# Kernel optimization log

Hardware: AMD Instinct MI355X
Metric: run time of the kernel (lower is better)

Reference implementation:

```python
import jax, jax.numpy as jnp
import numpy as np

GAMMA = 0.01   # module default gamma
STEP = 10      # forward subsamples time axis with x[::10]
BIG = 1e10     # finite stand-in for +inf boundary (exp(-BIG/gamma) underflows to 0 exactly)


def _softdtw(D, gamma):
    """Batched soft-DTW DP over cost matrices D: (B, N, M) -> (B,).
    Anti-diagonal wavefront: lax.scan over the 2*max(N,M)-1 diagonals,
    each diagonal updated fully vectorized (mirrors compute_softdtw_cuda).
    """
    B, N, M = D.shape
    inv_g = 1.0 / gamma
    # padded R, boundaries at BIG (acts as +inf), R[:,0,0] = 0
    R0 = jnp.full((B, N + 2, M + 2), BIG, dtype=D.dtype).at[:, 0, 0].set(0.0)
    ii = jnp.arange(1, N + 1)  # padded row indices on a diagonal

    def step(R, p):
        jj = p + 2 - ii                      # i + j = p + 2 in padded coords
        valid = (jj >= 1) & (jj <= M)
        jc = jnp.clip(jj, 1, M)
        r0 = -R[:, ii - 1, jc - 1] * inv_g   # diag neighbor
        r1 = -R[:, ii - 1, jc] * inv_g       # up neighbor
        r2 = -R[:, ii, jc - 1] * inv_g       # left neighbor
        rmax = jnp.maximum(jnp.maximum(r0, r1), r2)
        rsum = jnp.exp(r0 - rmax) + jnp.exp(r1 - rmax) + jnp.exp(r2 - rmax)
        softmin = -gamma * (jnp.log(rsum) + rmax)
        new = D[:, ii - 1, jc - 1] + softmin
        R = R.at[:, ii, jc].set(jnp.where(valid[None, :], new, R[:, ii, jc]))
        return R, None

    R, _ = jax.lax.scan(step, R0, jnp.arange(N + M - 1))
    return R[:, N, M]


def _loss(x, y):
    # x, y: (nt, nr, nc). Subsample time by STEP; treat each (r, c) trace as a
    # batch-1, dim-1 sequence; sum soft-DTW values over all nr*nc traces.
    xs = x[::STEP]                      # (L, nr, nc)
    ys = y[::STEP]
    L = xs.shape[0]
    X = xs.reshape(L, -1).T             # (B, L), B = nr*nc
    Y = ys.reshape(L, -1).T
    D = (X[:, :, None] - Y[:, None, :]) ** 2  # squared-Euclidean cost, d=1
    return jnp.sum(_softdtw(D, GAMMA)).reshape(1)


def setup_inputs() -> dict:
    key = jax.random.key(0)
    k1, k2 = jax.random.split(key)
    x = jax.random.normal(k1, (2048, 128, 2), dtype=jnp.float32)
    y = jax.random.normal(k2, (2048, 128, 2), dtype=jnp.float32)
    return {"x": x, "y": y}


def reference(x, y):
    return _loss(x, y)
```

## Files before the change

### kernel.cpp

```cpp
#include <hip/hip_runtime.h>

#define STEP 10
#define NCH  256
#define CSCL (-144.2695041f)
#define GLN2 (-0.00693147181f)
#define BIGP (-1.442695041e12f)
#define YOFF 64
#define YLDS 384
#define BNDSZ 472
#define NW   4

__device__ __forceinline__ float fexp2(float x){ float r; asm("v_exp_f32 %0, %1" : "=v"(r) : "v"(x)); return r; }
__device__ __forceinline__ float flog2(float x){ float r; asm("v_log_f32 %0, %1" : "=v"(r) : "v"(x)); return r; }

__device__ __forceinline__ float dpp_shr1(float src){
    int s = __builtin_bit_cast(int, src);
    int r = __builtin_amdgcn_update_dpp(0, s, 0x138 , 0xF, 0xF, true);
    return __builtin_bit_cast(float, r);
}

__device__ __forceinline__ float dpcell(float up2, float up, float left, float qq) {
    float m  = fmaxf(fmaxf(up2, up), left);
    float lo = fminf(fminf(up2, up), left);
    float md = __builtin_amdgcn_fmed3f(up2, up, left);
    float e  = fexp2(lo - m) + fexp2(md - m) + 1.0f;
    float mq = m + qq;
    return flog2(e) + mq;
}

__global__ __launch_bounds__(256, 1)
void softdtw_wave(const float* __restrict__ x, const float* __restrict__ y,
                  float* __restrict__ ws, int N) {
    const int b = blockIdx.x;
    const int t = threadIdx.x;
    const int l = t & 63;
    const int w = t >> 6;

    __shared__ __align__(16) float Ys[YLDS];
    __shared__ float bnd[NW - 1][BNDSZ];
    __shared__ int prog[NW - 1];

    for (int j = t; j < YLDS; j += 256) Ys[j] = 0.f;
    float* bf = &bnd[0][0];
    for (int j = t; j < (NW - 1) * BNDSZ; j += 256) bf[j] = BIGP;
    if (t < NW - 1) prog[t] = 0;
    __syncthreads();
    for (int j = t; j < N; j += 256) Ys[YOFF + j] = y[j * STEP * NCH + b];
    __syncthreads();

    const int i = 64 * w + l + 1;
    const float xv = (i <= N) ? x[(i - 1) * STEP * NCH + b] : 0.f;

    float sp = BIGP, bp = BIGP;
    float bq = (t == 0) ? 0.0f : BIGP;

    const int smax = 2 * N;
    const int sb0  = 64 * w + 2;
    const int myrows = (64 * (w + 1) < N) ? 64 * (w + 1) : N;
    const int NG     = (myrows + N - sb0 + 1 + 7) >> 3;
    const bool prod = (w < NW - 1);
    const bool cons = (w > 0);
    const int prows = (64 * w < N) ? 64 * w : N;
    const int pNG   = (prows + N - (sb0 - 64) + 1 + 7) >> 3;
    const int progFinal = (sb0 - 64) + 8 * pNG - 1;

    const float* yb = Ys + (YOFF - l);
    const float* bb = cons ? bnd[w - 1] : bnd[0];

    #define POLL(NEED) do {                                               \
        const int need_ = min((NEED), progFinal);                         \
        while (__hip_atomic_load(&prog[w - 1], __ATOMIC_ACQUIRE,          \
                                 __HIP_MEMORY_SCOPE_WORKGROUP) < need_)   \
            __builtin_amdgcn_s_sleep(1);                                  \
    } while (0)

    float q0,q1,q2,q3,q4,q5,q6,q7;
    float h0,h1,h2,h3,h4,h5,h6,h7;
    {
        float a0=yb[0],a1=yb[1],a2=yb[2],a3=yb[3];
        float a4=yb[4],a5=yb[5],a6=yb[6],a7=yb[7];
        if (cons) {
            POLL(sb0 + 7);
            if (l == 0) bp = bb[sb0 - 1];
            h0=bb[sb0+0]; h1=bb[sb0+1]; h2=bb[sb0+2]; h3=bb[sb0+3];
            h4=bb[sb0+4]; h5=bb[sb0+5]; h6=bb[sb0+6]; h7=bb[sb0+7];
        } else {
            h0=h1=h2=h3=h4=h5=h6=h7 = BIGP;
        }
        float d;
        d=xv-a0; q0=d*CSCL*d;  d=xv-a1; q1=d*CSCL*d;
        d=xv-a2; q2=d*CSCL*d;  d=xv-a3; q3=d*CSCL*d;
        d=xv-a4; q4=d*CSCL*d;  d=xv-a5; q5=d*CSCL*d;
        d=xv-a6; q6=d*CSCL*d;  d=xv-a7; q7=d*CSCL*d;
    }

    #define STEPJ(QQ, HJ, CJ, J) do {                              \
        CJ = dpcell(bq, bp, sp, (QQ));                             \
        float sh = dpp_shr1(CJ);                                   \
        bq = bp;                                                   \
        bp = (l == 0) ? (HJ) : sh;                                 \
        sp = CJ;                                                   \
        if (sb + (J) == smax && i == N) ws[b] = CJ * GLN2;         \
    } while (0)

    for (int m = 0; m < NG; ++m) {
        const int sb = sb0 + 8 * m;
        float c0,c1,c2,c3,c4,c5,c6,c7;
        STEPJ(q0, h0, c0, 0); STEPJ(q1, h1, c1, 1);
        STEPJ(q2, h2, c2, 2); STEPJ(q3, h3, c3, 3);
        STEPJ(q4, h4, c4, 4); STEPJ(q5, h5, c5, 5);
        STEPJ(q6, h6, c6, 6); STEPJ(q7, h7, c7, 7);

        if (prod && l == 63) {
            float* bw = &bnd[w][sb];
            bw[0]=c0; bw[1]=c1; bw[2]=c2; bw[3]=c3;
            bw[4]=c4; bw[5]=c5; bw[6]=c6; bw[7]=c7;
            __hip_atomic_store(&prog[w], sb + 7, __ATOMIC_RELEASE,
                               __HIP_MEMORY_SCOPE_WORKGROUP);
        }

        if (m + 1 < NG) {
            const float* yn = yb + 8 * (m + 1);
            float a0=yn[0],a1=yn[1],a2=yn[2],a3=yn[3];
            float a4=yn[4],a5=yn[5],a6=yn[6],a7=yn[7];
            if (cons) {
                POLL(sb + 15);
                h0=bb[sb+8];  h1=bb[sb+9];  h2=bb[sb+10]; h3=bb[sb+11];
                h4=bb[sb+12]; h5=bb[sb+13]; h6=bb[sb+14]; h7=bb[sb+15];
            }
            float d;
            d=xv-a0; q0=d*CSCL*d;  d=xv-a1; q1=d*CSCL*d;
            d=xv-a2; q2=d*CSCL*d;  d=xv-a3; q3=d*CSCL*d;
            d=xv-a4; q4=d*CSCL*d;  d=xv-a5; q5=d*CSCL*d;
            d=xv-a6; q6=d*CSCL*d;  d=xv-a7; q7=d*CSCL*d;
        }
    }
    #undef STEPJ
    #undef POLL
}

__global__ __launch_bounds__(256)
void reduce256(const float* __restrict__ ws, float* __restrict__ out) {
    const int tid = threadIdx.x;
    float v = ws[tid];
    #pragma unroll
    for (int off = 32; off > 0; off >>= 1)
        v += __shfl_down(v, off, 64);
    __shared__ float partial[4];
    if ((tid & 63) == 0) partial[tid >> 6] = v;
    __syncthreads();
    if (tid == 0) out[0] = (partial[0] + partial[1]) + (partial[2] + partial[3]);
}

extern "C" void kernel_launch(void* const* d_in, const int* in_sizes, int n_in,
                              void* d_out, int out_size, void* d_ws, size_t ws_size,
                              hipStream_t stream) {
    const float* x = (const float*)d_in[0];
    const float* y = (const float*)d_in[1];
    float* out = (float*)d_out;
    float* ws  = (float*)d_ws;

    const int T = in_sizes[0] / NCH;
    const int L = (T + STEP - 1) / STEP;

    softdtw_wave<<<dim3(NCH), dim3(256), 0, stream>>>(x, y, ws, L);
    reduce256<<<dim3(1), dim3(256), 0, stream>>>(ws, out);
}
```

Measured before the change: 38.17 us.

## Process two traces per block to interleave independent DP chains

Each workgroup now runs two independent soft-DTW problems (channels 2b and 2b+1) side by side, interleaving their per-cell computations so the serial exp/log/DPP dependency chain of one trace can overlap with the other. The grid halves to 128 blocks. The DPP shift now takes the lane-0 boundary value as its old operand, which removes a separate select. In exchange it uses twice the registers and LDS per block, and only 128 of the GPU's CUs get work.

```diff
diff --git a/kernel.cpp b/kernel.cpp
--- a/kernel.cpp
+++ b/kernel.cpp
@@ -13,9 +13,10 @@
 __device__ __forceinline__ float fexp2(float x){ float r; asm("v_exp_f32 %0, %1" : "=v"(r) : "v"(x)); return r; }
 __device__ __forceinline__ float flog2(float x){ float r; asm("v_log_f32 %0, %1" : "=v"(r) : "v"(x)); return r; }
 
-__device__ __forceinline__ float dpp_shr1(float src){
+__device__ __forceinline__ float dpp_shr1_sel(float h, float src){
+    int o = __builtin_bit_cast(int, h);
     int s = __builtin_bit_cast(int, src);
-    int r = __builtin_amdgcn_update_dpp(0, s, 0x138 , 0xF, 0xF, true);
+    int r = __builtin_amdgcn_update_dpp(o, s, 0x138 , 0xF, 0xF, false);
     return __builtin_bit_cast(float, r);
 }
 
@@ -31,28 +32,33 @@
 __global__ __launch_bounds__(256, 1)
 void softdtw_wave(const float* __restrict__ x, const float* __restrict__ y,
                   float* __restrict__ ws, int N) {
-    const int b = blockIdx.x;
+    const int bA = blockIdx.x * 2;
+    const int bB = bA + 1;
     const int t = threadIdx.x;
     const int l = t & 63;
     const int w = t >> 6;
 
-    __shared__ __align__(16) float Ys[YLDS];
-    __shared__ float bnd[NW - 1][BNDSZ];
+    __shared__ __align__(16) float YsA[YLDS], YsB[YLDS];
+    __shared__ float bndA[NW - 1][BNDSZ], bndB[NW - 1][BNDSZ];
     __shared__ int prog[NW - 1];
 
-    for (int j = t; j < YLDS; j += 256) Ys[j] = 0.f;
-    float* bf = &bnd[0][0];
-    for (int j = t; j < (NW - 1) * BNDSZ; j += 256) bf[j] = BIGP;
+    for (int j = t; j < YLDS; j += 256) { YsA[j] = 0.f; YsB[j] = 0.f; }
+    float* bfA = &bndA[0][0]; float* bfB = &bndB[0][0];
+    for (int j = t; j < (NW - 1) * BNDSZ; j += 256) { bfA[j] = BIGP; bfB[j] = BIGP; }
     if (t < NW - 1) prog[t] = 0;
     __syncthreads();
-    for (int j = t; j < N; j += 256) Ys[YOFF + j] = y[j * STEP * NCH + b];
+    for (int j = t; j < N; j += 256) {
+        YsA[YOFF + j] = y[j * STEP * NCH + bA];
+        YsB[YOFF + j] = y[j * STEP * NCH + bB];
+    }
     __syncthreads();
 
     const int i = 64 * w + l + 1;
-    const float xv = (i <= N) ? x[(i - 1) * STEP * NCH + b] : 0.f;
-
-    float sp = BIGP, bp = BIGP;
-    float bq = (t == 0) ? 0.0f : BIGP;
+    const float xvA = (i <= N) ? x[(i - 1) * STEP * NCH + bA] : 0.f;
+    const float xvB = (i <= N) ? x[(i - 1) * STEP * NCH + bB] : 0.f;
+
+    float spA = BIGP, bpA = BIGP, bqA = (t == 0) ? 0.0f : BIGP;
+    float spB = BIGP, bpB = BIGP, bqB = (t == 0) ? 0.0f : BIGP;
 
     const int smax = 2 * N;
     const int sb0  = 64 * w + 2;
@@ -64,8 +70,10 @@
     const int pNG   = (prows + N - (sb0 - 64) + 1 + 7) >> 3;
     const int progFinal = (sb0 - 64) + 8 * pNG - 1;
 
-    const float* yb = Ys + (YOFF - l);
-    const float* bb = cons ? bnd[w - 1] : bnd[0];
+    const float* ybA = YsA + (YOFF - l);
+    const float* ybB = YsB + (YOFF - l);
+    const float* bbA = cons ? bndA[w - 1] : bndA[0];
+    const float* bbB = cons ? bndB[w - 1] : bndB[0];
 
     #define POLL(NEED) do {                                               \
         const int need_ = min((NEED), progFinal);                         \
@@ -74,68 +82,97 @@
             __builtin_amdgcn_s_sleep(1);                                  \
     } while (0)
 
-    float q0,q1,q2,q3,q4,q5,q6,q7;
-    float h0,h1,h2,h3,h4,h5,h6,h7;
+    float qA0,qA1,qA2,qA3,qA4,qA5,qA6,qA7, qB0,qB1,qB2,qB3,qB4,qB5,qB6,qB7;
+    float hA0,hA1,hA2,hA3,hA4,hA5,hA6,hA7, hB0,hB1,hB2,hB3,hB4,hB5,hB6,hB7;
     {
-        float a0=yb[0],a1=yb[1],a2=yb[2],a3=yb[3];
-        float a4=yb[4],a5=yb[5],a6=yb[6],a7=yb[7];
+        float a0=ybA[0],a1=ybA[1],a2=ybA[2],a3=ybA[3];
+        float a4=ybA[4],a5=ybA[5],a6=ybA[6],a7=ybA[7];
+        float e0=ybB[0],e1=ybB[1],e2=ybB[2],e3=ybB[3];
+        float e4=ybB[4],e5=ybB[5],e6=ybB[6],e7=ybB[7];
         if (cons) {
             POLL(sb0 + 7);
-            if (l == 0) bp = bb[sb0 - 1];
-            h0=bb[sb0+0]; h1=bb[sb0+1]; h2=bb[sb0+2]; h3=bb[sb0+3];
-            h4=bb[sb0+4]; h5=bb[sb0+5]; h6=bb[sb0+6]; h7=bb[sb0+7];
+            if (l == 0) { bpA = bbA[sb0 - 1]; bpB = bbB[sb0 - 1]; }
+            hA0=bbA[sb0+0]; hA1=bbA[sb0+1]; hA2=bbA[sb0+2]; hA3=bbA[sb0+3];
+            hA4=bbA[sb0+4]; hA5=bbA[sb0+5]; hA6=bbA[sb0+6]; hA7=bbA[sb0+7];
+            hB0=bbB[sb0+0]; hB1=bbB[sb0+1]; hB2=bbB[sb0+2]; hB3=bbB[sb0+3];
+            hB4=bbB[sb0+4]; hB5=bbB[sb0+5]; hB6=bbB[sb0+6]; hB7=bbB[sb0+7];
         } else {
-            h0=h1=h2=h3=h4=h5=h6=h7 = BIGP;
+            hA0=hA1=hA2=hA3=hA4=hA5=hA6=hA7 = BIGP;
+            hB0=hB1=hB2=hB3=hB4=hB5=hB6=hB7 = BIGP;
         }
         float d;
-        d=xv-a0; q0=d*CSCL*d;  d=xv-a1; q1=d*CSCL*d;
-        d=xv-a2; q2=d*CSCL*d;  d=xv-a3; q3=d*CSCL*d;
-        d=xv-a4; q4=d*CSCL*d;  d=xv-a5; q5=d*CSCL*d;
-        d=xv-a6; q6=d*CSCL*d;  d=xv-a7; q7=d*CSCL*d;
+        d=xvA-a0; qA0=d*CSCL*d;  d=xvA-a1; qA1=d*CSCL*d;
+        d=xvA-a2; qA2=d*CSCL*d;  d=xvA-a3; qA3=d*CSCL*d;
+        d=xvA-a4; qA4=d*CSCL*d;  d=xvA-a5; qA5=d*CSCL*d;
+        d=xvA-a6; qA6=d*CSCL*d;  d=xvA-a7; qA7=d*CSCL*d;
+        d=xvB-e0; qB0=d*CSCL*d;  d=xvB-e1; qB1=d*CSCL*d;
+        d=xvB-e2; qB2=d*CSCL*d;  d=xvB-e3; qB3=d*CSCL*d;
+        d=xvB-e4; qB4=d*CSCL*d;  d=xvB-e5; qB5=d*CSCL*d;
+        d=xvB-e6; qB6=d*CSCL*d;  d=xvB-e7; qB7=d*CSCL*d;
     }
 
-    #define STEPJ(QQ, HJ, CJ, J) do {                              \
-        CJ = dpcell(bq, bp, sp, (QQ));                             \
-        float sh = dpp_shr1(CJ);                                   \
-        bq = bp;                                                   \
-        bp = (l == 0) ? (HJ) : sh;                                 \
-        sp = CJ;                                                   \
-        if (sb + (J) == smax && i == N) ws[b] = CJ * GLN2;         \
+    #define STEPJ2(QA, HA, CA, QB, HB, CB, J) do {                 \
+        CA = dpcell(bqA, bpA, spA, (QA));                          \
+        CB = dpcell(bqB, bpB, spB, (QB));                          \
+        float nA = dpp_shr1_sel((HA), CA);                         \
+        float nB = dpp_shr1_sel((HB), CB);                         \
+        bqA = bpA; bpA = nA; spA = CA;                             \
+        bqB = bpB; bpB = nB; spB = CB;                             \
+        if (sb + (J) == smax && i == N) {                          \
+            ws[bA] = CA * GLN2; ws[bB] = CB * GLN2;                \
+        }                                                          \
     } while (0)
 
     for (int m = 0; m < NG; ++m) {
         const int sb = sb0 + 8 * m;
-        float c0,c1,c2,c3,c4,c5,c6,c7;
-        STEPJ(q0, h0, c0, 0); STEPJ(q1, h1, c1, 1);
-        STEPJ(q2, h2, c2, 2); STEPJ(q3, h3, c3, 3);
-        STEPJ(q4, h4, c4, 4); STEPJ(q5, h5, c5, 5);
-        STEPJ(q6, h6, c6, 6); STEPJ(q7, h7, c7, 7);
+        float cA0,cA1,cA2,cA3,cA4,cA5,cA6,cA7;
+        float cB0,cB1,cB2,cB3,cB4,cB5,cB6,cB7;
+        STEPJ2(qA0,hA0,cA0, qB0,hB0,cB0, 0);
+        STEPJ2(qA1,hA1,cA1, qB1,hB1,cB1, 1);
+        STEPJ2(qA2,hA2,cA2, qB2,hB2,cB2, 2);
+        STEPJ2(qA3,hA3,cA3, qB3,hB3,cB3, 3);
+        STEPJ2(qA4,hA4,cA4, qB4,hB4,cB4, 4);
+        STEPJ2(qA5,hA5,cA5, qB5,hB5,cB5, 5);
+        STEPJ2(qA6,hA6,cA6, qB6,hB6,cB6, 6);
+        STEPJ2(qA7,hA7,cA7, qB7,hB7,cB7, 7);
 
         if (prod && l == 63) {
-            float* bw = &bnd[w][sb];
-            bw[0]=c0; bw[1]=c1; bw[2]=c2; bw[3]=c3;
-            bw[4]=c4; bw[5]=c5; bw[6]=c6; bw[7]=c7;
+            float* bwA = &bndA[w][sb];
+            bwA[0]=cA0; bwA[1]=cA1; bwA[2]=cA2; bwA[3]=cA3;
+            bwA[4]=cA4; bwA[5]=cA5; bwA[6]=cA6; bwA[7]=cA7;
+            float* bwB = &bndB[w][sb];
+            bwB[0]=cB0; bwB[1]=cB1; bwB[2]=cB2; bwB[3]=cB3;
+            bwB[4]=cB4; bwB[5]=cB5; bwB[6]=cB6; bwB[7]=cB7;
             __hip_atomic_store(&prog[w], sb + 7, __ATOMIC_RELEASE,
                                __HIP_MEMORY_SCOPE_WORKGROUP);
         }
 
         if (m + 1 < NG) {
-            const float* yn = yb + 8 * (m + 1);
-            float a0=yn[0],a1=yn[1],a2=yn[2],a3=yn[3];
-            float a4=yn[4],a5=yn[5],a6=yn[6],a7=yn[7];
+            const float* ynA = ybA + 8 * (m + 1);
+            const float* ynB = ybB + 8 * (m + 1);
+            float a0=ynA[0],a1=ynA[1],a2=ynA[2],a3=ynA[3];
+            float a4=ynA[4],a5=ynA[5],a6=ynA[6],a7=ynA[7];
+            float e0=ynB[0],e1=ynB[1],e2=ynB[2],e3=ynB[3];
+            float e4=ynB[4],e5=ynB[5],e6=ynB[6],e7=ynB[7];
             if (cons) {
                 POLL(sb + 15);
-                h0=bb[sb+8];  h1=bb[sb+9];  h2=bb[sb+10]; h3=bb[sb+11];
-                h4=bb[sb+12]; h5=bb[sb+13]; h6=bb[sb+14]; h7=bb[sb+15];
+                hA0=bbA[sb+8];  hA1=bbA[sb+9];  hA2=bbA[sb+10]; hA3=bbA[sb+11];
+                hA4=bbA[sb+12]; hA5=bbA[sb+13]; hA6=bbA[sb+14]; hA7=bbA[sb+15];
+                hB0=bbB[sb+8];  hB1=bbB[sb+9];  hB2=bbB[sb+10]; hB3=bbB[sb+11];
+                hB4=bbB[sb+12]; hB5=bbB[sb+13]; hB6=bbB[sb+14]; hB7=bbB[sb+15];
             }
             float d;
-            d=xv-a0; q0=d*CSCL*d;  d=xv-a1; q1=d*CSCL*d;
-            d=xv-a2; q2=d*CSCL*d;  d=xv-a3; q3=d*CSCL*d;
-            d=xv-a4; q4=d*CSCL*d;  d=xv-a5; q5=d*CSCL*d;
-            d=xv-a6; q6=d*CSCL*d;  d=xv-a7; q7=d*CSCL*d;
+            d=xvA-a0; qA0=d*CSCL*d;  d=xvA-a1; qA1=d*CSCL*d;
+            d=xvA-a2; qA2=d*CSCL*d;  d=xvA-a3; qA3=d*CSCL*d;
+            d=xvA-a4; qA4=d*CSCL*d;  d=xvA-a5; qA5=d*CSCL*d;
+            d=xvA-a6; qA6=d*CSCL*d;  d=xvA-a7; qA7=d*CSCL*d;
+            d=xvB-e0; qB0=d*CSCL*d;  d=xvB-e1; qB1=d*CSCL*d;
+            d=xvB-e2; qB2=d*CSCL*d;  d=xvB-e3; qB3=d*CSCL*d;
+            d=xvB-e4; qB4=d*CSCL*d;  d=xvB-e5; qB5=d*CSCL*d;
+            d=xvB-e6; qB6=d*CSCL*d;  d=xvB-e7; qB7=d*CSCL*d;
         }
     }
-    #undef STEPJ
+    #undef STEPJ2
     #undef POLL
 }
 
@@ -163,6 +200,6 @@
     const int T = in_sizes[0] / NCH;
     const int L = (T + STEP - 1) / STEP;
 
-    softdtw_wave<<<dim3(NCH), dim3(256), 0, stream>>>(x, y, ws, L);
+    softdtw_wave<<<dim3(NCH / 2), dim3(256), 0, stream>>>(x, y, ws, L);
     reduce256<<<dim3(1), dim3(256), 0, stream>>>(ws, out);
 }
```

Measured after the change: 53.72 us. +40.7%, slower.

## Double-buffer boundary/Y loads, fold reduction into last block, early progress signals

Applied to the files above, without the earlier changes.

The DP loop is unrolled by two with ping-pong register sets, so Y values and boundary values for the next group are loaded while the current group computes, and the cost term is computed inline per cell. The DPP shift now takes the boundary value as its 'old' operand with bound_ctrl off, which removes the lane-0 select. Producers publish progress before writing their boundary values, and a sentinel is set at the end. The separate reduction kernel is replaced by an atomic counter where the last block sums the results, which adds a memset launch. The early progress store may let consumers read before the data is written, since the index it publishes looks like it refers only to earlier, already-written groups.

```diff
diff --git a/kernel.cpp b/kernel.cpp
--- a/kernel.cpp
+++ b/kernel.cpp
@@ -13,9 +13,10 @@
 __device__ __forceinline__ float fexp2(float x){ float r; asm("v_exp_f32 %0, %1" : "=v"(r) : "v"(x)); return r; }
 __device__ __forceinline__ float flog2(float x){ float r; asm("v_log_f32 %0, %1" : "=v"(r) : "v"(x)); return r; }
 
-__device__ __forceinline__ float dpp_shr1(float src){
+__device__ __forceinline__ float dpp_shr1_sel(float h, float src){
+    int o = __builtin_bit_cast(int, h);
     int s = __builtin_bit_cast(int, src);
-    int r = __builtin_amdgcn_update_dpp(0, s, 0x138 , 0xF, 0xF, true);
+    int r = __builtin_amdgcn_update_dpp(o, s, 0x138 , 0xF, 0xF, false);
     return __builtin_bit_cast(float, r);
 }
 
@@ -28,9 +29,14 @@
     return flog2(e) + mq;
 }
 
+#define PIN8(A0,A1,A2,A3,A4,A5,A6,A7) \
+    asm volatile("" : "+v"(A0),"+v"(A1),"+v"(A2),"+v"(A3), \
+                      "+v"(A4),"+v"(A5),"+v"(A6),"+v"(A7))
+
 __global__ __launch_bounds__(256, 1)
 void softdtw_wave(const float* __restrict__ x, const float* __restrict__ y,
-                  float* __restrict__ ws, int N) {
+                  float* __restrict__ ws, int* __restrict__ cnt,
+                  float* __restrict__ out, int N) {
     const int b = blockIdx.x;
     const int t = threadIdx.x;
     const int l = t & 63;
@@ -39,6 +45,8 @@
     __shared__ __align__(16) float Ys[YLDS];
     __shared__ float bnd[NW - 1][BNDSZ];
     __shared__ int prog[NW - 1];
+    __shared__ float res_s;
+    __shared__ int last_s;
 
     for (int j = t; j < YLDS; j += 256) Ys[j] = 0.f;
     float* bf = &bnd[0][0];
@@ -64,7 +72,7 @@
     const int pNG   = (prows + N - (sb0 - 64) + 1 + 7) >> 3;
     const int progFinal = (sb0 - 64) + 8 * pNG - 1;
 
-    const float* yb = Ys + (YOFF - l);
+    const float* yrow = Ys + (YOFF - l);
     const float* bb = cons ? bnd[w - 1] : bnd[0];
 
     #define POLL(NEED) do {                                               \
@@ -74,82 +82,135 @@
             __builtin_amdgcn_s_sleep(1);                                  \
     } while (0)
 
-    float q0,q1,q2,q3,q4,q5,q6,q7;
-    float h0,h1,h2,h3,h4,h5,h6,h7;
-    {
-        float a0=yb[0],a1=yb[1],a2=yb[2],a3=yb[3];
-        float a4=yb[4],a5=yb[5],a6=yb[6],a7=yb[7];
-        if (cons) {
-            POLL(sb0 + 7);
-            if (l == 0) bp = bb[sb0 - 1];
-            h0=bb[sb0+0]; h1=bb[sb0+1]; h2=bb[sb0+2]; h3=bb[sb0+3];
-            h4=bb[sb0+4]; h5=bb[sb0+5]; h6=bb[sb0+6]; h7=bb[sb0+7];
-        } else {
-            h0=h1=h2=h3=h4=h5=h6=h7 = BIGP;
+    float ya0,ya1,ya2,ya3,ya4,ya5,ya6,ya7, hb0,hb1,hb2,hb3,hb4,hb5,hb6,hb7;
+    float yB0,yB1,yB2,yB3,yB4,yB5,yB6,yB7, ha0,ha1,ha2,ha3,ha4,ha5,ha6,ha7;
+    ya0=yrow[0]; ya1=yrow[1]; ya2=yrow[2]; ya3=yrow[3];
+    ya4=yrow[4]; ya5=yrow[5]; ya6=yrow[6]; ya7=yrow[7];
+    yB0=yrow[8]; yB1=yrow[9]; yB2=yrow[10]; yB3=yrow[11];
+    yB4=yrow[12]; yB5=yrow[13]; yB6=yrow[14]; yB7=yrow[15];
+    if (cons) {
+        POLL(sb0 + 15);
+        if (l == 0) bp = bb[sb0 - 1];
+        ha0=bb[sb0+0]; ha1=bb[sb0+1]; ha2=bb[sb0+2]; ha3=bb[sb0+3];
+        ha4=bb[sb0+4]; ha5=bb[sb0+5]; ha6=bb[sb0+6]; ha7=bb[sb0+7];
+        hb0=bb[sb0+8]; hb1=bb[sb0+9]; hb2=bb[sb0+10]; hb3=bb[sb0+11];
+        hb4=bb[sb0+12]; hb5=bb[sb0+13]; hb6=bb[sb0+14]; hb7=bb[sb0+15];
+    } else {
+        ha0=ha1=ha2=ha3=ha4=ha5=ha6=ha7 = BIGP;
+        hb0=hb1=hb2=hb3=hb4=hb5=hb6=hb7 = BIGP;
+    }
+    PIN8(ya0,ya1,ya2,ya3,ya4,ya5,ya6,ya7);
+    PIN8(ha0,ha1,ha2,ha3,ha4,ha5,ha6,ha7);
+
+    #define STEPJ(YV, HJ, CJ, J) do {                              \
+        float d_ = xv - (YV);                                      \
+        float q_ = d_ * CSCL * d_;                                 \
+        CJ = dpcell(bq, bp, sp, q_);                               \
+        float n_ = dpp_shr1_sel((HJ), CJ);                         \
+        bq = bp; bp = n_; sp = CJ;                                 \
+        if (sb + (J) == smax && i == N) res_s = CJ * GLN2;         \
+    } while (0)
+
+    int m = 0;
+    for (; m + 1 < NG; m += 2) {
+        {
+            const int sb = sb0 + 8 * m;
+            float c0,c1,c2,c3,c4,c5,c6,c7;
+            STEPJ(ya0,ha0,c0,0); STEPJ(ya1,ha1,c1,1);
+            STEPJ(ya2,ha2,c2,2); STEPJ(ya3,ha3,c3,3);
+            STEPJ(ya4,ha4,c4,4); STEPJ(ya5,ha5,c5,5);
+            STEPJ(ya6,ha6,c6,6); STEPJ(ya7,ha7,c7,7);
+            if (prod && l == 63) {
+                __hip_atomic_store(&prog[w], sb - 1, __ATOMIC_RELEASE,
+                                   __HIP_MEMORY_SCOPE_WORKGROUP);
+                float* bw = &bnd[w][sb];
+                bw[0]=c0; bw[1]=c1; bw[2]=c2; bw[3]=c3;
+                bw[4]=c4; bw[5]=c5; bw[6]=c6; bw[7]=c7;
+            }
+            if (m + 2 < NG) {
+                if (cons) {
+                    POLL(sb0 + 8*(m+2) + 7);
+                    const float* hh = &bb[sb0 + 8*(m+2)];
+                    ha0=hh[0]; ha1=hh[1]; ha2=hh[2]; ha3=hh[3];
+                    ha4=hh[4]; ha5=hh[5]; ha6=hh[6]; ha7=hh[7];
+                }
+                const float* yn = yrow + 8*(m+2);
+                ya0=yn[0]; ya1=yn[1]; ya2=yn[2]; ya3=yn[3];
+                ya4=yn[4]; ya5=yn[5]; ya6=yn[6]; ya7=yn[7];
+            }
+            PIN8(yB0,yB1,yB2,yB3,yB4,yB5,yB6,yB7);
+            PIN8(hb0,hb1,hb2,hb3,hb4,hb5,hb6,hb7);
         }
-        float d;
-        d=xv-a0; q0=d*CSCL*d;  d=xv-a1; q1=d*CSCL*d;
-        d=xv-a2; q2=d*CSCL*d;  d=xv-a3; q3=d*CSCL*d;
-        d=xv-a4; q4=d*CSCL*d;  d=xv-a5; q5=d*CSCL*d;
-        d=xv-a6; q6=d*CSCL*d;  d=xv-a7; q7=d*CSCL*d;
-    }
-
-    #define STEPJ(QQ, HJ, CJ, J) do {                              \
-        CJ = dpcell(bq, bp, sp, (QQ));                             \
-        float sh = dpp_shr1(CJ);                                   \
-        bq = bp;                                                   \
-        bp = (l == 0) ? (HJ) : sh;                                 \
-        sp = CJ;                                                   \
-        if (sb + (J) == smax && i == N) ws[b] = CJ * GLN2;         \
-    } while (0)
-
-    for (int m = 0; m < NG; ++m) {
+        {
+            const int sb = sb0 + 8 * (m + 1);
+            float c0,c1,c2,c3,c4,c5,c6,c7;
+            STEPJ(yB0,hb0,c0,0); STEPJ(yB1,hb1,c1,1);
+            STEPJ(yB2,hb2,c2,2); STEPJ(yB3,hb3,c3,3);
+            STEPJ(yB4,hb4,c4,4); STEPJ(yB5,hb5,c5,5);
+            STEPJ(yB6,hb6,c6,6); STEPJ(yB7,hb7,c7,7);
+            if (prod && l == 63) {
+                __hip_atomic_store(&prog[w], sb - 1, __ATOMIC_RELEASE,
+                                   __HIP_MEMORY_SCOPE_WORKGROUP);
+                float* bw = &bnd[w][sb];
+                bw[0]=c0; bw[1]=c1; bw[2]=c2; bw[3]=c3;
+                bw[4]=c4; bw[5]=c5; bw[6]=c6; bw[7]=c7;
+            }
+            if (m + 3 < NG) {
+                if (cons) {
+                    POLL(sb0 + 8*(m+3) + 7);
+                    const float* hh = &bb[sb0 + 8*(m+3)];
+                    hb0=hh[0]; hb1=hh[1]; hb2=hh[2]; hb3=hh[3];
+                    hb4=hh[4]; hb5=hh[5]; hb6=hh[6]; hb7=hh[7];
+                }
+                const float* yn = yrow + 8*(m+3);
+                yB0=yn[0]; yB1=yn[1]; yB2=yn[2]; yB3=yn[3];
+                yB4=yn[4]; yB5=yn[5]; yB6=yn[6]; yB7=yn[7];
+            }
+            PIN8(ya0,ya1,ya2,ya3,ya4,ya5,ya6,ya7);
+            PIN8(ha0,ha1,ha2,ha3,ha4,ha5,ha6,ha7);
+        }
+    }
+    if (m < NG) {
         const int sb = sb0 + 8 * m;
         float c0,c1,c2,c3,c4,c5,c6,c7;
-        STEPJ(q0, h0, c0, 0); STEPJ(q1, h1, c1, 1);
-        STEPJ(q2, h2, c2, 2); STEPJ(q3, h3, c3, 3);
-        STEPJ(q4, h4, c4, 4); STEPJ(q5, h5, c5, 5);
-        STEPJ(q6, h6, c6, 6); STEPJ(q7, h7, c7, 7);
-
+        STEPJ(ya0,ha0,c0,0); STEPJ(ya1,ha1,c1,1);
+        STEPJ(ya2,ha2,c2,2); STEPJ(ya3,ha3,c3,3);
+        STEPJ(ya4,ha4,c4,4); STEPJ(ya5,ha5,c5,5);
+        STEPJ(ya6,ha6,c6,6); STEPJ(ya7,ha7,c7,7);
         if (prod && l == 63) {
+            __hip_atomic_store(&prog[w], sb - 1, __ATOMIC_RELEASE,
+                               __HIP_MEMORY_SCOPE_WORKGROUP);
             float* bw = &bnd[w][sb];
             bw[0]=c0; bw[1]=c1; bw[2]=c2; bw[3]=c3;
             bw[4]=c4; bw[5]=c5; bw[6]=c6; bw[7]=c7;
-            __hip_atomic_store(&prog[w], sb + 7, __ATOMIC_RELEASE,
-                               __HIP_MEMORY_SCOPE_WORKGROUP);
         }
-
-        if (m + 1 < NG) {
-            const float* yn = yb + 8 * (m + 1);
-            float a0=yn[0],a1=yn[1],a2=yn[2],a3=yn[3];
-            float a4=yn[4],a5=yn[5],a6=yn[6],a7=yn[7];
-            if (cons) {
-                POLL(sb + 15);
-                h0=bb[sb+8];  h1=bb[sb+9];  h2=bb[sb+10]; h3=bb[sb+11];
-                h4=bb[sb+12]; h5=bb[sb+13]; h6=bb[sb+14]; h7=bb[sb+15];
-            }
-            float d;
-            d=xv-a0; q0=d*CSCL*d;  d=xv-a1; q1=d*CSCL*d;
-            d=xv-a2; q2=d*CSCL*d;  d=xv-a3; q3=d*CSCL*d;
-            d=xv-a4; q4=d*CSCL*d;  d=xv-a5; q5=d*CSCL*d;
-            d=xv-a6; q6=d*CSCL*d;  d=xv-a7; q7=d*CSCL*d;
-        }
-    }
+    }
+    if (prod && l == 63)
+        __hip_atomic_store(&prog[w], 0x3FFFFFFF, __ATOMIC_RELEASE,
+                           __HIP_MEMORY_SCOPE_WORKGROUP);
     #undef STEPJ
     #undef POLL
-}
-
-__global__ __launch_bounds__(256)
-void reduce256(const float* __restrict__ ws, float* __restrict__ out) {
-    const int tid = threadIdx.x;
-    float v = ws[tid];
-    #pragma unroll
-    for (int off = 32; off > 0; off >>= 1)
-        v += __shfl_down(v, off, 64);
-    __shared__ float partial[4];
-    if ((tid & 63) == 0) partial[tid >> 6] = v;
-    __syncthreads();
-    if (tid == 0) out[0] = (partial[0] + partial[1]) + (partial[2] + partial[3]);
+
+    __syncthreads();
+    if (t == 0) {
+        __hip_atomic_store(&ws[b], res_s, __ATOMIC_RELEASE,
+                           __HIP_MEMORY_SCOPE_AGENT);
+        int prev = __hip_atomic_fetch_add(cnt, 1, __ATOMIC_ACQ_REL,
+                                          __HIP_MEMORY_SCOPE_AGENT);
+        last_s = (prev == NCH - 1);
+    }
+    __syncthreads();
+    if (last_s) {
+        float v = __hip_atomic_load(&ws[t], __ATOMIC_RELAXED,
+                                    __HIP_MEMORY_SCOPE_AGENT);
+        #pragma unroll
+        for (int off = 32; off > 0; off >>= 1)
+            v += __shfl_down(v, off, 64);
+        __shared__ float partial[4];
+        if ((t & 63) == 0) partial[t >> 6] = v;
+        __syncthreads();
+        if (t == 0) out[0] = (partial[0] + partial[1]) + (partial[2] + partial[3]);
+    }
 }
 
 extern "C" void kernel_launch(void* const* d_in, const int* in_sizes, int n_in,
@@ -159,10 +220,11 @@
     const float* y = (const float*)d_in[1];
     float* out = (float*)d_out;
     float* ws  = (float*)d_ws;
+    int*   cnt = (int*)(ws + NCH);
 
     const int T = in_sizes[0] / NCH;
     const int L = (T + STEP - 1) / STEP;
 
-    softdtw_wave<<<dim3(NCH), dim3(256), 0, stream>>>(x, y, ws, L);
-    reduce256<<<dim3(1), dim3(256), 0, stream>>>(ws, out);
-}
+    hipMemsetAsync(cnt, 0, sizeof(int), stream);
+    softdtw_wave<<<dim3(NCH), dim3(256), 0, stream>>>(x, y, ws, cnt, out, L);
+}
```

Measured after the change: 48.26 us. +26.4%, slower.

## Split soft-DTW rows across eight waves of 26 rows each

Applied to the files above, without the earlier changes.

The wavefront pipeline goes from 4 waves of 64 rows to 8 waves per block, each owning a 26-row stripe. Stripes are mapped so consecutive stages sit on different SIMDs. The lane-0 boundary select is folded into the DPP move by using the old-value operand with bound_ctrl off, which removes a per-cell v_cndmask. The goal is a shorter critical path: less pipeline fill per stage and fewer serial cells per wave, at the cost of more producer/consumer handoffs and idle lanes (38 of 64 lanes do redundant work).

```diff
diff --git a/kernel.cpp b/kernel.cpp
--- a/kernel.cpp
+++ b/kernel.cpp
@@ -7,15 +7,17 @@
 #define BIGP (-1.442695041e12f)
 #define YOFF 64
 #define YLDS 384
-#define BNDSZ 472
-#define NW   4
+#define BNDSZ 424
+#define NWAVE 8
+#define SROW 26
 
 __device__ __forceinline__ float fexp2(float x){ float r; asm("v_exp_f32 %0, %1" : "=v"(r) : "v"(x)); return r; }
 __device__ __forceinline__ float flog2(float x){ float r; asm("v_log_f32 %0, %1" : "=v"(r) : "v"(x)); return r; }
 
-__device__ __forceinline__ float dpp_shr1(float src){
+__device__ __forceinline__ float dpp_shr1_sel(float h, float src){
+    int o = __builtin_bit_cast(int, h);
     int s = __builtin_bit_cast(int, src);
-    int r = __builtin_amdgcn_update_dpp(0, s, 0x138 , 0xF, 0xF, true);
+    int r = __builtin_amdgcn_update_dpp(o, s, 0x138 , 0xF, 0xF, false);
     return __builtin_bit_cast(float, r);
 }
 
@@ -28,48 +30,51 @@
     return flog2(e) + mq;
 }
 
-__global__ __launch_bounds__(256, 1)
+__global__ __launch_bounds__(512, 1)
 void softdtw_wave(const float* __restrict__ x, const float* __restrict__ y,
                   float* __restrict__ ws, int N) {
     const int b = blockIdx.x;
     const int t = threadIdx.x;
     const int l = t & 63;
     const int w = t >> 6;
+    const int stg = ((w & 3) << 1) | (w >> 2);
 
     __shared__ __align__(16) float Ys[YLDS];
-    __shared__ float bnd[NW - 1][BNDSZ];
-    __shared__ int prog[NW - 1];
+    __shared__ float bnd[NWAVE - 1][BNDSZ];
+    __shared__ int prog[NWAVE - 1];
 
-    for (int j = t; j < YLDS; j += 256) Ys[j] = 0.f;
+    for (int j = t; j < YLDS; j += 512) Ys[j] = 0.f;
     float* bf = &bnd[0][0];
-    for (int j = t; j < (NW - 1) * BNDSZ; j += 256) bf[j] = BIGP;
-    if (t < NW - 1) prog[t] = 0;
+    for (int j = t; j < (NWAVE - 1) * BNDSZ; j += 512) bf[j] = BIGP;
+    if (t < NWAVE - 1) prog[t] = 0;
     __syncthreads();
-    for (int j = t; j < N; j += 256) Ys[YOFF + j] = y[j * STEP * NCH + b];
+    for (int j = t; j < N; j += 512) Ys[YOFF + j] = y[j * STEP * NCH + b];
     __syncthreads();
 
-    const int i = 64 * w + l + 1;
+    const int off = SROW * stg;
+    const int i = off + l + 1;
     const float xv = (i <= N) ? x[(i - 1) * STEP * NCH + b] : 0.f;
 
     float sp = BIGP, bp = BIGP;
-    float bq = (t == 0) ? 0.0f : BIGP;
+    float bq = (stg == 0 && l == 0) ? 0.0f : BIGP;
 
     const int smax = 2 * N;
-    const int sb0  = 64 * w + 2;
-    const int myrows = (64 * (w + 1) < N) ? 64 * (w + 1) : N;
-    const int NG     = (myrows + N - sb0 + 1 + 7) >> 3;
-    const bool prod = (w < NW - 1);
-    const bool cons = (w > 0);
-    const int prows = (64 * w < N) ? 64 * w : N;
-    const int pNG   = (prows + N - (sb0 - 64) + 1 + 7) >> 3;
-    const int progFinal = (sb0 - 64) + 8 * pNG - 1;
+    const int sb0  = off + 2;
+    const int myLast = ((off + SROW < N) ? off + SROW : N) + N;
+    const int NG     = (myLast - sb0 + 1 + 7) >> 3;
+    const bool prod = (stg < NWAVE - 1);
+    const bool cons = (stg > 0);
+    const int pLast = ((off < N) ? off : N) + N;
+    const int psb0  = off - SROW + 2;
+    const int pNG   = (pLast - psb0 + 1 + 7) >> 3;
+    const int progFinal = psb0 + 8 * pNG - 1;
 
-    const float* yb = Ys + (YOFF - l);
-    const float* bb = cons ? bnd[w - 1] : bnd[0];
+    const float* yrow = Ys + (YOFF - l);
+    const float* bb = cons ? bnd[stg - 1] : bnd[0];
 
     #define POLL(NEED) do {                                               \
         const int need_ = min((NEED), progFinal);                         \
-        while (__hip_atomic_load(&prog[w - 1], __ATOMIC_ACQUIRE,          \
+        while (__hip_atomic_load(&prog[stg - 1], __ATOMIC_ACQUIRE,        \
                                  __HIP_MEMORY_SCOPE_WORKGROUP) < need_)   \
             __builtin_amdgcn_s_sleep(1);                                  \
     } while (0)
@@ -77,8 +82,8 @@
     float q0,q1,q2,q3,q4,q5,q6,q7;
     float h0,h1,h2,h3,h4,h5,h6,h7;
     {
-        float a0=yb[0],a1=yb[1],a2=yb[2],a3=yb[3];
-        float a4=yb[4],a5=yb[5],a6=yb[6],a7=yb[7];
+        float a0=yrow[0],a1=yrow[1],a2=yrow[2],a3=yrow[3];
+        float a4=yrow[4],a5=yrow[5],a6=yrow[6],a7=yrow[7];
         if (cons) {
             POLL(sb0 + 7);
             if (l == 0) bp = bb[sb0 - 1];
@@ -96,11 +101,10 @@
 
     #define STEPJ(QQ, HJ, CJ, J) do {                              \
         CJ = dpcell(bq, bp, sp, (QQ));                             \
-        float sh = dpp_shr1(CJ);                                   \
-        bq = bp;                                                   \
-        bp = (l == 0) ? (HJ) : sh;                                 \
-        sp = CJ;                                                   \
-        if (sb + (J) == smax && i == N) ws[b] = CJ * GLN2;         \
+        float n_ = dpp_shr1_sel((HJ), CJ);                         \
+        bq = bp; bp = n_; sp = CJ;                                 \
+        if (sb + (J) == smax && i == N && stg == NWAVE - 1)        \
+            ws[b] = CJ * GLN2;                                     \
     } while (0)
 
     for (int m = 0; m < NG; ++m) {
@@ -111,16 +115,16 @@
         STEPJ(q4, h4, c4, 4); STEPJ(q5, h5, c5, 5);
         STEPJ(q6, h6, c6, 6); STEPJ(q7, h7, c7, 7);
 
-        if (prod && l == 63) {
-            float* bw = &bnd[w][sb];
+        if (prod && l == SROW - 1) {
+            float* bw = &bnd[stg][sb];
             bw[0]=c0; bw[1]=c1; bw[2]=c2; bw[3]=c3;
             bw[4]=c4; bw[5]=c5; bw[6]=c6; bw[7]=c7;
-            __hip_atomic_store(&prog[w], sb + 7, __ATOMIC_RELEASE,
+            __hip_atomic_store(&prog[stg], sb + 7, __ATOMIC_RELEASE,
                                __HIP_MEMORY_SCOPE_WORKGROUP);
         }
 
         if (m + 1 < NG) {
-            const float* yn = yb + 8 * (m + 1);
+            const float* yn = yrow + 8 * (m + 1);
             float a0=yn[0],a1=yn[1],a2=yn[2],a3=yn[3];
             float a4=yn[4],a5=yn[5],a6=yn[6],a7=yn[7];
             if (cons) {
@@ -163,6 +167,6 @@
     const int T = in_sizes[0] / NCH;
     const int L = (T + STEP - 1) / STEP;
 
-    softdtw_wave<<<dim3(NCH), dim3(256), 0, stream>>>(x, y, ws, L);
+    softdtw_wave<<<dim3(NCH), dim3(512), 0, stream>>>(x, y, ws, L);
     reduce256<<<dim3(1), dim3(256), 0, stream>>>(ws, out);
 }
```

Result: slower. 57.37 us (+50.3%).
